# Performance work log

Measured on AMD Instinct MI355X. Metric: run time of the kernel, lower is better.

Reference implementation:

```python
import jax, jax.numpy as jnp
import numpy as np

B, T, D = 4, 8192, 512
H, BS = 8, 16


def setup_inputs() -> dict:
    key = jax.random.key(0)
    ks = jax.random.split(key, 7)
    s = 1.0 / np.sqrt(D)
    return {
        "x": jax.random.normal(ks[0], (B, T, D), dtype=jnp.float32),
        "Wq": jax.random.normal(ks[1], (D, D), dtype=jnp.float32) * s,
        "bq": jax.random.normal(ks[2], (D,), dtype=jnp.float32) * 0.02,
        "Wk": jax.random.normal(ks[3], (D, D), dtype=jnp.float32) * s,
        "bk": jax.random.normal(ks[4], (D,), dtype=jnp.float32) * 0.02,
        "Wv": jax.random.normal(ks[5], (D, D), dtype=jnp.float32) * s,
        "bv": jax.random.normal(ks[6], (D,), dtype=jnp.float32) * 0.02,
    }


def reference(x, Wq, bq, Wk, bk, Wv, bv):
    b, t, d_model = x.shape
    nb = t // BS          # number of blocks
    dh = d_model // H     # per-head dim
    # [B,T,D] -> [B,nb,BS,D] -> [B,BS,nb,D]: attention runs across blocks
    xb = x.reshape(b, nb, BS, d_model).transpose(0, 2, 1, 3)
    # projections (torch Linear: x @ W.T + b)
    q = xb @ Wq.T + bq
    k = xb @ Wk.T + bk
    v = xb @ Wv.T + bv
    # split heads: [B,BS,nb,H,dh] -> [B,BS,H,nb,dh]
    q = q.reshape(b, BS, nb, H, dh).transpose(0, 1, 3, 2, 4)
    k = k.reshape(b, BS, nb, H, dh).transpose(0, 1, 3, 2, 4)
    v = v.reshape(b, BS, nb, H, dh).transpose(0, 1, 3, 2, 4)
    scale = d_model ** (-0.5)  # note: full dim, as in the original
    attn = jnp.einsum('bshnd,bshmd->bshnm', q, k) * scale  # [B,BS,H,nb,nb]
    attn = jax.nn.softmax(attn, axis=-1)
    out = jnp.einsum('bshnm,bshmd->bshnd', attn, v)        # [B,BS,H,nb,dh]
    # merge heads and undo block permute
    out = out.transpose(0, 1, 3, 2, 4).reshape(b, BS, nb, d_model)
    out = out.transpose(0, 2, 1, 3).reshape(b, t, d_model)
    return out
```

## Files before the change

kernel.cpp:

```cpp
#include <hip/hip_runtime.h>
#include <hip/hip_bf16.h>
#include <cstdint>
#include <cstddef>

#define Bsz 4
#define Tsz 8192
#define Dsz 512
#define Hn 8
#define BSn 16
#define NBn 512
#define DHn 64
#define NQKV 1536
#define MROWS 32768

#define SCL 0.06375870136f
#define ATT_M 8.0f

typedef __attribute__((ext_vector_type(8))) short short8;
typedef __attribute__((ext_vector_type(4))) float float4f;

__device__ __forceinline__ uint16_t f2b(float f) {
  union { float f; uint32_t u; } v; v.f = f;
  uint32_t u = v.u;
  return (uint16_t)((u + 0x7fffu + ((u >> 16) & 1u)) >> 16);
}

__device__ __forceinline__ uint32_t pk2t(float a, float b) {
  union { float f; uint32_t u; } x, y; x.f = a; y.f = b;
  return __builtin_amdgcn_perm(y.u, x.u, 0x07060302u);
}

__device__ __forceinline__ void gl_lds16(const void* g, void* l) {
  __builtin_amdgcn_global_load_lds(
      (const __attribute__((address_space(1))) unsigned int*)g,
      (__attribute__((address_space(3))) unsigned int*)l, 16, 0, 0);
}

#define XBLK (MROWS * Dsz / 1024)
__global__ void cvt_kernel(const float* __restrict__ x, const float* __restrict__ Wq,
                           const float* __restrict__ Wk, const float* __restrict__ Wv,
                           uint16_t* __restrict__ xb, uint16_t* __restrict__ wc) {
  int bid = blockIdx.x;
  if (bid < XBLK) {
    int i = (bid * 256 + threadIdx.x) * 4;
    float4 v = *(const float4*)(x + i);
    union { uint16_t u16[4]; uint64_t u64; } o;
    o.u16[0] = f2b(v.x); o.u16[1] = f2b(v.y); o.u16[2] = f2b(v.z); o.u16[3] = f2b(v.w);
    *(uint64_t*)(xb + i) = o.u64;
  } else {
    int i = ((bid - XBLK) * 256 + threadIdx.x) * 4;
    int row = i >> 9;
    int col = i & 511;
    const float* src = (row < 512) ? Wq : ((row < 1024) ? Wk : Wv);
    float4 v = *(const float4*)(src + (size_t)(row & 511) * 512 + col);
    union { uint16_t u16[4]; uint64_t u64; } o;
    o.u16[0] = f2b(v.x); o.u16[1] = f2b(v.y); o.u16[2] = f2b(v.z); o.u16[3] = f2b(v.w);
    *(uint64_t*)(wc + i) = o.u64;
  }
}

#define BM 128
#define BN 128
#define BK 64

__global__ __launch_bounds__(256) void gemm_qkv(
    const uint16_t* __restrict__ Xb, const uint16_t* __restrict__ Wc,
    const float* __restrict__ bq, const float* __restrict__ bkp,
    const float* __restrict__ bv, uint16_t* __restrict__ Qp,
    uint16_t* __restrict__ Kp, uint16_t* __restrict__ Vtmp) {
  __shared__ uint16_t As[BM * BK];
  __shared__ uint16_t Bs[BN * BK];
  const int tid = threadIdx.x;
  const int wave = tid >> 6, lane = tid & 63;
  const int lrow = lane & 15, quad = lane >> 4;

  int g = blockIdx.x;
  int xcd = g & 7, ii = g >> 3;
  int mt = xcd * 32 + ii / 12;
  int nt = ii - (ii / 12) * 12;
  const int m0 = mt * BM;
  const int n0 = nt * BN;
  const int wm = (wave >> 1) * 64, wn = (wave & 1) * 64;

  float4f acc[4][4] = {};

  for (int k0 = 0; k0 < Dsz; k0 += BK) {
    __syncthreads();
#pragma unroll
    for (int p = 0; p < 4; ++p) {
      int cbase = p * 256 + wave * 64;
      int c = cbase + lane;
      int row = c >> 3, pos = c & 7;
      int kc = (pos ^ (row & 7)) * 8;
      gl_lds16(Xb + (size_t)(m0 + row) * Dsz + k0 + kc, As + cbase * 8);
      gl_lds16(Wc + (size_t)(n0 + row) * Dsz + k0 + kc, Bs + cbase * 8);
    }
    __syncthreads();

#pragma unroll
    for (int h = 0; h < 2; ++h) {
      short8 af[4], bf[4];
#pragma unroll
      for (int i = 0; i < 4; ++i) {
        int rowA = wm + i * 16 + lrow;
        af[i] = *(const short8*)(As + rowA * BK + (((h * 4 + quad) ^ (rowA & 7)) * 8));
        int rowB = wn + i * 16 + lrow;
        bf[i] = *(const short8*)(Bs + rowB * BK + (((h * 4 + quad) ^ (rowB & 7)) * 8));
      }
#pragma unroll
      for (int i = 0; i < 4; ++i)
#pragma unroll
        for (int j = 0; j < 4; ++j)
          acc[i][j] = __builtin_amdgcn_mfma_f32_16x16x32_bf16(af[i], bf[j], acc[i][j], 0, 0, 0);
    }
  }

  const int region = n0 >> 9;
  const float* bias = (region == 0) ? bq : ((region == 1) ? bkp : bv);
  const float mult = (region == 0) ? SCL : 1.0f;
  const int bb = m0 >> 13;
  const int nbbase = ((m0 & 8191) >> 4) + (wm >> 4);

  if (region < 2) {
    uint16_t* dst = (region == 0) ? Qp : Kp;
#pragma unroll
    for (int j = 0; j < 4; ++j) {
      int nl = (n0 + wn + j * 16 + lrow) & 511;
      int hh = nl >> 6, dh = nl & 63;
      float bval = bias[nl];
      size_t base = (size_t)bb * 4194304 + (size_t)hh * 32768 +
                    (size_t)nbbase * 64 + dh + (size_t)(quad * 4) * 262144;
#pragma unroll
      for (int i = 0; i < 4; ++i)
#pragma unroll
        for (int r = 0; r < 4; ++r)
          dst[base + (size_t)r * 262144 + (size_t)i * 64] =
              f2b((acc[i][j][r] + bval) * mult);
    }
  } else {
#pragma unroll
    for (int j = 0; j < 4; ++j) {
      int nl = (n0 + wn + j * 16 + lrow) & 511;
      float bval = bias[nl];
#pragma unroll
      for (int i = 0; i < 4; ++i) {
        int tok = m0 + wm + i * 16 + quad * 4;
#pragma unroll
        for (int r = 0; r < 4; ++r)
          Vtmp[(size_t)(tok + r) * 512 + nl] = f2b(acc[i][j][r] + bval);
      }
    }
  }
}

__global__ __launch_bounds__(256) void vtrans(const uint16_t* __restrict__ Vtmp,
                                              uint16_t* __restrict__ Vt) {
  __shared__ uint16_t tile[64 * 64];
  int bx = blockIdx.x;
  const int nt = bx & 7; bx >>= 3;
  const int h = bx & 7; bx >>= 3;
  const int s = bx & 15;
  const int b = bx >> 4;
  const int tid = threadIdx.x;

  {
    int i = tid >> 2;
    int token = b * Tsz + (nt * 64 + i) * BSn + s;
    const uint16_t* src = Vtmp + (size_t)token * 512 + h * 64;
#pragma unroll
    for (int hh = 0; hh < 2; ++hh) {
      int ch = (tid & 3) * 2 + hh;
      short8 v = *(const short8*)(src + ch * 8);
      int pc = ch ^ (i & 7);
      *(short8*)(tile + i * 64 + pc * 8) = v;
    }
  }
  __syncthreads();
  {
    int dh = tid & 63, seg = tid >> 6;
    short8 v1, v2;
#pragma unroll
    for (int k = 0; k < 8; ++k) {
      int nb_l = seg * 16 + k;
      v1[k] = (short)tile[nb_l * 64 + (((dh >> 3) ^ (nb_l & 7)) * 8) + (dh & 7)];
    }
#pragma unroll
    for (int k = 0; k < 8; ++k) {
      int nb_l = seg * 16 + 8 + k;
      v2[k] = (short)tile[nb_l * 64 + (((dh >> 3) ^ (nb_l & 7)) * 8) + (dh & 7)];
    }
    size_t obase = ((((size_t)b * 16 + s) * 8 + h) * 64 + dh) * 512 + nt * 64 + seg * 16;
    *(short8*)(Vt + obase) = v1;
    *(short8*)(Vt + obase + 8) = v2;
  }
}

__global__ __launch_bounds__(256, 3) void attn_kernel(
    const uint16_t* __restrict__ Qp, const uint16_t* __restrict__ Kp,
    const uint16_t* __restrict__ Vt, float* __restrict__ out) {
  __shared__ uint16_t Ks[32 * 64];
  __shared__ uint16_t Vs[64 * 32];
  __shared__ uint16_t Ps[4][4][16 * 32];

  int bx = blockIdx.x;
  const int qh = bx & 1; bx >>= 1;
  const int h = bx & 7; bx >>= 3;
  const int s = bx & 15;
  const int b = bx >> 4;

  const int tid = threadIdx.x;
  const int w = tid >> 6, lane = tid & 63;
  const int lrow = lane & 15, quad = lane >> 4;

  const size_t sh = (((size_t)b * 16 + s) * 8 + h);
  const uint16_t* Qb = Qp + (sh << 15);
  const uint16_t* Kb = Kp + (sh << 15);
  const uint16_t* Vb = Vt + (sh << 15);

  short8 qB[4][2];
  const int q0 = qh * 256 + w * 64;
#pragma unroll
  for (int qs = 0; qs < 4; ++qs) {
    const uint16_t* qp = Qb + (size_t)(q0 + qs * 16 + lrow) * 64;
    qB[qs][0] = *(const short8*)(qp + quad * 8);
    qB[qs][1] = *(const short8*)(qp + 32 + quad * 8);
  }

  float4f O[4][4] = {};
  float l_acc[4] = {0.f, 0.f, 0.f, 0.f};

  const int kr = w * 8 + (lane >> 3);
  const int kcs = (lane & 7) ^ (kr & 7);
  const int vr = w * 16 + (lane >> 2);
  const int vcs = (lane & 3) ^ ((vr >> 1) & 3);

  const int sw = (lrow >> 1) & 3;

  for (int kv0 = 0; kv0 < NBn; kv0 += 32) {
    __syncthreads();
    gl_lds16(Kb + (size_t)(kv0 + kr) * 64 + kcs * 8, Ks + w * 512);
    gl_lds16(Vb + (size_t)vr * 512 + kv0 + vcs * 8, Vs + w * 512);
    __syncthreads();

    {
      short8 kA[2][2];
#pragma unroll
      for (int kt = 0; kt < 2; ++kt) {
        int row = kt * 16 + lrow;
#pragma unroll
        for (int kc = 0; kc < 2; ++kc) {
          int cc = (kc * 4 + quad) ^ (row & 7);
          kA[kt][kc] = *(const short8*)(Ks + row * 64 + cc * 8);
        }
      }
#pragma unroll
      for (int qs = 0; qs < 4; ++qs) {
        float4f c0 = {}, c1 = {};
        c0 = __builtin_amdgcn_mfma_f32_16x16x32_bf16(kA[0][0], qB[qs][0], c0, 0, 0, 0);
        c0 = __builtin_amdgcn_mfma_f32_16x16x32_bf16(kA[0][1], qB[qs][1], c0, 0, 0, 0);
        c1 = __builtin_amdgcn_mfma_f32_16x16x32_bf16(kA[1][0], qB[qs][0], c1, 0, 0, 0);
        c1 = __builtin_amdgcn_mfma_f32_16x16x32_bf16(kA[1][1], qB[qs][1], c1, 0, 0, 0);

        float p00 = __builtin_amdgcn_exp2f(c0[0] - ATT_M);
        float p01 = __builtin_amdgcn_exp2f(c0[1] - ATT_M);
        float p02 = __builtin_amdgcn_exp2f(c0[2] - ATT_M);
        float p03 = __builtin_amdgcn_exp2f(c0[3] - ATT_M);
        float p10 = __builtin_amdgcn_exp2f(c1[0] - ATT_M);
        float p11 = __builtin_amdgcn_exp2f(c1[1] - ATT_M);
        float p12 = __builtin_amdgcn_exp2f(c1[2] - ATT_M);
        float p13 = __builtin_amdgcn_exp2f(c1[3] - ATT_M);
        l_acc[qs] += ((p00 + p01) + (p02 + p03)) + ((p10 + p11) + (p12 + p13));

        uint32_t d0 = pk2t(p00, p01), d1 = pk2t(p02, p03);
        uint32_t d2 = pk2t(p10, p11), d3 = pk2t(p12, p13);
        uint16_t* Psq = Ps[w][qs];
        int half = (quad & 1) * 4;
        *(uint2*)(Psq + lrow * 32 + (((quad >> 1)) ^ sw) * 8 + half) = make_uint2(d0, d1);
        *(uint2*)(Psq + lrow * 32 + ((2 + (quad >> 1)) ^ sw) * 8 + half) = make_uint2(d2, d3);
      }
    }

    {
      short8 vA[4];
#pragma unroll
      for (int dt = 0; dt < 4; ++dt) {
        int row = dt * 16 + lrow;
        vA[dt] = *(const short8*)(Vs + row * 32 + (quad ^ ((row >> 1) & 3)) * 8);
      }
#pragma unroll
      for (int qs = 0; qs < 4; ++qs) {
        short8 pB = *(const short8*)(Ps[w][qs] + lrow * 32 + (quad ^ sw) * 8);
#pragma unroll
        for (int dt = 0; dt < 4; ++dt)
          O[dt][qs] = __builtin_amdgcn_mfma_f32_16x16x32_bf16(vA[dt], pB, O[dt][qs], 0, 0, 0);
      }
    }
  }

#pragma unroll
  for (int qs = 0; qs < 4; ++qs) {
    float l = l_acc[qs];
    l += __shfl_xor(l, 16);
    l += __shfl_xor(l, 32);
    float inv = 1.0f / l;
    int qg = q0 + qs * 16 + lrow;
    float* op = out + ((size_t)b * Tsz + (size_t)qg * 16 + s) * Dsz + h * 64;
#pragma unroll
    for (int dt = 0; dt < 4; ++dt) {
      float4 vv;
      vv.x = O[dt][qs][0] * inv; vv.y = O[dt][qs][1] * inv;
      vv.z = O[dt][qs][2] * inv; vv.w = O[dt][qs][3] * inv;
      *(float4*)(op + dt * 16 + quad * 4) = vv;
    }
  }
}

extern "C" void kernel_launch(void* const* d_in, const int* in_sizes, int n_in,
                              void* d_out, int out_size, void* d_ws, size_t ws_size,
                              hipStream_t stream) {
  const float* x  = (const float*)d_in[0];
  const float* Wq = (const float*)d_in[1];
  const float* bq = (const float*)d_in[2];
  const float* Wk = (const float*)d_in[3];
  const float* bk = (const float*)d_in[4];
  const float* Wv = (const float*)d_in[5];
  const float* bv = (const float*)d_in[6];
  float* out = (float*)d_out;

  uint16_t* Qp   = (uint16_t*)d_ws;
  uint16_t* Kp   = Qp + (size_t)16777216;
  uint16_t* Vtmp = Kp + (size_t)16777216;
  uint16_t* xb   = Vtmp + (size_t)16777216;
  uint16_t* wc   = xb + (size_t)16777216;
  uint16_t* Vt   = xb;

  hipLaunchKernelGGL(cvt_kernel, dim3(XBLK + NQKV * Dsz / 1024), dim3(256), 0, stream,
                     x, Wq, Wk, Wv, xb, wc);
  hipLaunchKernelGGL(gemm_qkv, dim3((MROWS / BM) * (NQKV / BN)), dim3(256), 0, stream,
                     xb, wc, bq, bk, bv, Qp, Kp, Vtmp);
  hipLaunchKernelGGL(vtrans, dim3(Bsz * BSn * Hn * 8), dim3(256), 0, stream, Vtmp, Vt);
  hipLaunchKernelGGL(attn_kernel, dim3(Bsz * BSn * Hn * 2), dim3(256), 0, stream,
                     Qp, Kp, Vt, out);
}
```

Baseline: 270.9 us.

## Transpose QKV GEMM MFMA operands for vectorized epilogue stores and fold softmax offset

Swaps the A/B operands of the QKV GEMM MFMA so each lane holds four consecutive output columns. This lets the epilogue write packed 8-byte bf16 stores with float4 bias loads instead of scattered 2-byte stores. It also replaces the round-to-nearest-even bf16 conversion with a cheaper round-half-up pack in the convert kernel and epilogue, and folds the fixed softmax offset into the MFMA accumulator initialisation. The rounding change slightly alters numerics, and the transposed accumulator indexing must match the new store layout.

Result: slower. 277.1 us (+2.3%).

```diff
diff --git a/kernel.cpp b/kernel.cpp
--- a/kernel.cpp
+++ b/kernel.cpp
@@ -25,6 +25,11 @@
   return (uint16_t)((u + 0x7fffu + ((u >> 16) & 1u)) >> 16);
 }
 
+__device__ __forceinline__ uint32_t pk2(float a, float b) {
+  union { float f; uint32_t u; } x, y; x.f = a; y.f = b;
+  return __builtin_amdgcn_perm(y.u + 0x8000u, x.u + 0x8000u, 0x07060302u);
+}
+
 __device__ __forceinline__ uint32_t pk2t(float a, float b) {
   union { float f; uint32_t u; } x, y; x.f = a; y.f = b;
   return __builtin_amdgcn_perm(y.u, x.u, 0x07060302u);
@@ -44,18 +49,16 @@
   if (bid < XBLK) {
     int i = (bid * 256 + threadIdx.x) * 4;
     float4 v = *(const float4*)(x + i);
-    union { uint16_t u16[4]; uint64_t u64; } o;
-    o.u16[0] = f2b(v.x); o.u16[1] = f2b(v.y); o.u16[2] = f2b(v.z); o.u16[3] = f2b(v.w);
-    *(uint64_t*)(xb + i) = o.u64;
+    uint64_t o = (uint64_t)pk2(v.x, v.y) | ((uint64_t)pk2(v.z, v.w) << 32);
+    *(uint64_t*)(xb + i) = o;
   } else {
     int i = ((bid - XBLK) * 256 + threadIdx.x) * 4;
     int row = i >> 9;
     int col = i & 511;
     const float* src = (row < 512) ? Wq : ((row < 1024) ? Wk : Wv);
     float4 v = *(const float4*)(src + (size_t)(row & 511) * 512 + col);
-    union { uint16_t u16[4]; uint64_t u64; } o;
-    o.u16[0] = f2b(v.x); o.u16[1] = f2b(v.y); o.u16[2] = f2b(v.z); o.u16[3] = f2b(v.w);
-    *(uint64_t*)(wc + i) = o.u64;
+    uint64_t o = (uint64_t)pk2(v.x, v.y) | ((uint64_t)pk2(v.z, v.w) << 32);
+    *(uint64_t*)(wc + i) = o;
   }
 }
 
@@ -108,10 +111,10 @@
         bf[i] = *(const short8*)(Bs + rowB * BK + (((h * 4 + quad) ^ (rowB & 7)) * 8));
       }
 #pragma unroll
-      for (int i = 0; i < 4; ++i)
-#pragma unroll
-        for (int j = 0; j < 4; ++j)
-          acc[i][j] = __builtin_amdgcn_mfma_f32_16x16x32_bf16(af[i], bf[j], acc[i][j], 0, 0, 0);
+      for (int j = 0; j < 4; ++j)
+#pragma unroll
+        for (int i = 0; i < 4; ++i)
+          acc[j][i] = __builtin_amdgcn_mfma_f32_16x16x32_bf16(bf[j], af[i], acc[j][i], 0, 0, 0);
     }
   }
 
@@ -120,34 +123,36 @@
   const float mult = (region == 0) ? SCL : 1.0f;
   const int bb = m0 >> 13;
   const int nbbase = ((m0 & 8191) >> 4) + (wm >> 4);
+  const int nv0 = (n0 & 511) + wn;
 
   if (region < 2) {
     uint16_t* dst = (region == 0) ? Qp : Kp;
+    const int hh = nv0 >> 6;
+    uint16_t* plane = dst + ((((size_t)bb * 16 + lrow) * 8 + hh) << 15);
 #pragma unroll
     for (int j = 0; j < 4; ++j) {
-      int nl = (n0 + wn + j * 16 + lrow) & 511;
-      int hh = nl >> 6, dh = nl & 63;
-      float bval = bias[nl];
-      size_t base = (size_t)bb * 4194304 + (size_t)hh * 32768 +
-                    (size_t)nbbase * 64 + dh + (size_t)(quad * 4) * 262144;
-#pragma unroll
-      for (int i = 0; i < 4; ++i)
-#pragma unroll
-        for (int r = 0; r < 4; ++r)
-          dst[base + (size_t)r * 262144 + (size_t)i * 64] =
-              f2b((acc[i][j][r] + bval) * mult);
+      int dh0 = j * 16 + quad * 4;
+      float4 bv4 = *(const float4*)(bias + nv0 + dh0);
+#pragma unroll
+      for (int i = 0; i < 4; ++i) {
+        float4f a = acc[j][i];
+        uint2 st = make_uint2(pk2((a[0] + bv4.x) * mult, (a[1] + bv4.y) * mult),
+                              pk2((a[2] + bv4.z) * mult, (a[3] + bv4.w) * mult));
+        *(uint2*)(plane + (size_t)(nbbase + i) * 64 + dh0) = st;
+      }
     }
   } else {
 #pragma unroll
     for (int j = 0; j < 4; ++j) {
-      int nl = (n0 + wn + j * 16 + lrow) & 511;
-      float bval = bias[nl];
+      int c0 = nv0 + j * 16 + quad * 4;
+      float4 bv4 = *(const float4*)(bias + c0);
 #pragma unroll
       for (int i = 0; i < 4; ++i) {
-        int tok = m0 + wm + i * 16 + quad * 4;
-#pragma unroll
-        for (int r = 0; r < 4; ++r)
-          Vtmp[(size_t)(tok + r) * 512 + nl] = f2b(acc[i][j][r] + bval);
+        int token = m0 + wm + i * 16 + lrow;
+        float4f a = acc[j][i];
+        uint2 st = make_uint2(pk2(a[0] + bv4.x, a[1] + bv4.y),
+                              pk2(a[2] + bv4.z, a[3] + bv4.w));
+        *(uint2*)(Vtmp + (size_t)token * 512 + c0) = st;
       }
     }
   }
@@ -235,6 +240,7 @@
   const int vcs = (lane & 3) ^ ((vr >> 1) & 3);
 
   const int sw = (lrow >> 1) & 3;
+  const float4f negm = {-ATT_M, -ATT_M, -ATT_M, -ATT_M};
 
   for (int kv0 = 0; kv0 < NBn; kv0 += 32) {
     __syncthreads();
@@ -255,20 +261,20 @@
       }
 #pragma unroll
       for (int qs = 0; qs < 4; ++qs) {
-        float4f c0 = {}, c1 = {};
+        float4f c0 = negm, c1 = negm;
         c0 = __builtin_amdgcn_mfma_f32_16x16x32_bf16(kA[0][0], qB[qs][0], c0, 0, 0, 0);
         c0 = __builtin_amdgcn_mfma_f32_16x16x32_bf16(kA[0][1], qB[qs][1], c0, 0, 0, 0);
         c1 = __builtin_amdgcn_mfma_f32_16x16x32_bf16(kA[1][0], qB[qs][0], c1, 0, 0, 0);
         c1 = __builtin_amdgcn_mfma_f32_16x16x32_bf16(kA[1][1], qB[qs][1], c1, 0, 0, 0);
 
-        float p00 = __builtin_amdgcn_exp2f(c0[0] - ATT_M);
-        float p01 = __builtin_amdgcn_exp2f(c0[1] - ATT_M);
-        float p02 = __builtin_amdgcn_exp2f(c0[2] - ATT_M);
-        float p03 = __builtin_amdgcn_exp2f(c0[3] - ATT_M);
-        float p10 = __builtin_amdgcn_exp2f(c1[0] - ATT_M);
-        float p11 = __builtin_amdgcn_exp2f(c1[1] - ATT_M);
-        float p12 = __builtin_amdgcn_exp2f(c1[2] - ATT_M);
-        float p13 = __builtin_amdgcn_exp2f(c1[3] - ATT_M);
+        float p00 = __builtin_amdgcn_exp2f(c0[0]);
+        float p01 = __builtin_amdgcn_exp2f(c0[1]);
+        float p02 = __builtin_amdgcn_exp2f(c0[2]);
+        float p03 = __builtin_amdgcn_exp2f(c0[3]);
+        float p10 = __builtin_amdgcn_exp2f(c1[0]);
+        float p11 = __builtin_amdgcn_exp2f(c1[1]);
+        float p12 = __builtin_amdgcn_exp2f(c1[2]);
+        float p13 = __builtin_amdgcn_exp2f(c1[3]);
         l_acc[qs] += ((p00 + p01) + (p02 + p03)) + ((p10 + p11) + (p12 + p13));
 
         uint32_t d0 = pk2t(p00, p01), d1 = pk2t(p02, p03);
```
